# Performance work log

Hardware: AMD Instinct MI355X
Metric: run time of the kernel (lower is better)

## Reference

```python
import jax, jax.numpy as jnp
import numpy as np

D_MODEL = 1024
N_HEADS = 16
D_K = D_MODEL // N_HEADS
WINDOW = 512
ROPE_BASE = 10000.0


def _apply_rope(x):
    # x: [B, H, S, D] ; torchtune-style interleaved-pair RoPE
    S, D = x.shape[2], x.shape[3]
    half = D // 2
    inv_freq = 1.0 / (ROPE_BASE ** (jnp.arange(half, dtype=jnp.float32) / half))
    ang = jnp.arange(S, dtype=jnp.float32)[:, None] * inv_freq[None, :]  # [S, half]
    cos = jnp.cos(ang).astype(x.dtype)  # [S, half]
    sin = jnp.sin(ang).astype(x.dtype)
    x_even = x[..., ::2]   # [B,H,S,half]
    x_odd = x[..., 1::2]
    out_even = x_even * cos - x_odd * sin
    out_odd = x_odd * cos + x_even * sin
    return jnp.stack([out_even, out_odd], axis=-1).reshape(x.shape)


def setup_inputs() -> dict:
    key = jax.random.key(0)
    k1, k2, k3 = jax.random.split(key, 3)
    B, S = 2, 2048
    x = jax.random.normal(k1, (B, S, D_MODEL), dtype=jnp.float32)
    # store weights pre-transposed so y = x @ w (same math as nn.Linear)
    w_qkv = jax.random.normal(k2, (D_MODEL, 3 * D_MODEL), dtype=jnp.float32) * (D_MODEL ** -0.5)
    w_o = jax.random.normal(k3, (D_MODEL, D_MODEL), dtype=jnp.float32) * (D_MODEL ** -0.5)
    return {"x": x, "w_qkv": w_qkv, "w_o": w_o}


def reference(x, w_qkv, w_o):
    B, S, _ = x.shape
    qkv = (x @ w_qkv).reshape(B, S, 3, N_HEADS, D_K)
    qkv = jnp.transpose(qkv, (2, 0, 3, 1, 4))  # [3, B, H, S, Dk]
    q, k, v = qkv[0], qkv[1], qkv[2]
    q = _apply_rope(q)
    k = _apply_rope(k)
    # causal sliding-window mask: token i attends to j in [i - WINDOW, i]
    i = jnp.arange(S)[:, None]
    j = jnp.arange(S)[None, :]
    allowed = (j <= i) & (j >= i - WINDOW)
    bias = jnp.where(allowed, 0.0, -jnp.inf).astype(x.dtype)  # [S, S]
    scores = jnp.einsum('bhqd,bhkd->bhqk', q, k) * (D_K ** -0.5) + bias
    attn = jax.nn.softmax(scores, axis=-1)
    out = jnp.einsum('bhqk,bhkd->bhqd', attn, v)  # [B,H,S,Dk]
    out = jnp.transpose(out, (0, 2, 1, 3)).reshape(B, S, D_MODEL)
    return out @ w_o
```

## Files before the change

### kernel.cpp

```cpp
#include <hip/hip_runtime.h>
#include <hip/hip_bf16.h>
#include <math.h>

typedef __bf16 bhalf;
typedef __bf16 bhalf8 __attribute__((ext_vector_type(8)));
typedef float floatx4 __attribute__((ext_vector_type(4)));
typedef _Float16 fh;
typedef _Float16 half4 __attribute__((ext_vector_type(4)));

#define MFMA_BF16(A, B, C) __builtin_amdgcn_mfma_f32_16x16x32_bf16((A), (B), (C), 0, 0, 0)
#define MFMA_F16_K16(A, B, C) __builtin_amdgcn_mfma_f32_16x16x16f16((A), (B), (C), 0, 0, 0)

__device__ inline unsigned short bfb(float f) {
  union { bhalf h; unsigned short u; } c;
  c.h = (bhalf)f;
  return c.u;
}
__device__ inline unsigned short fhb(float f) {
  union { fh h; unsigned short u; } c;
  c.h = (fh)f;
  return c.u;
}

__device__ inline void gload_lds16(const void* g, void* l) {
  typedef const __attribute__((address_space(1))) unsigned int GU;
  typedef __attribute__((address_space(3))) unsigned int LU;
  __builtin_amdgcn_global_load_lds((GU*)g, (LU*)l, 16, 0, 0);
}

__global__ __launch_bounds__(256) void cvt_x_kernel(const float* __restrict__ in,
                                                    bhalf* __restrict__ out) {
  int i = (blockIdx.x * 256 + threadIdx.x) * 8;
  floatx4 v0 = *(const floatx4*)(in + i);
  floatx4 v1 = *(const floatx4*)(in + i + 4);
  bhalf8 o;
  o[0] = (bhalf)v0[0]; o[1] = (bhalf)v0[1]; o[2] = (bhalf)v0[2]; o[3] = (bhalf)v0[3];
  o[4] = (bhalf)v1[0]; o[5] = (bhalf)v1[1]; o[6] = (bhalf)v1[2]; o[7] = (bhalf)v1[3];
  *(bhalf8*)(out + i) = o;
}

__global__ __launch_bounds__(256) void transpose_bf_kernel(const float* __restrict__ in,
                                                           bhalf* __restrict__ out,
                                                           int R, int C) {
  __shared__ float tile[32][33];
  int c0 = blockIdx.x * 32, r0 = blockIdx.y * 32;
  int tx = threadIdx.x, ty = threadIdx.y;
#pragma unroll
  for (int i = 0; i < 32; i += 8)
    tile[ty + i][tx] = in[(size_t)(r0 + ty + i) * C + c0 + tx];
  __syncthreads();
#pragma unroll
  for (int i = 0; i < 32; i += 8)
    out[(size_t)(c0 + ty + i) * R + r0 + tx] = (bhalf)tile[tx][ty + i];
}

template <int EPI, int TN>
__global__ __launch_bounds__(256, 2) void gemm_bt_kernel(
    const bhalf* __restrict__ A, const bhalf* __restrict__ BT, float* __restrict__ Cout,
    bhalf* __restrict__ qb, bhalf* __restrict__ kb, fh* __restrict__ vb,
    int M, int N, int K) {
  constexpr int NT = TN / 32;
  __shared__ __attribute__((aligned(16))) bhalf As[128 * 32];
  __shared__ __attribute__((aligned(16))) bhalf Bs[TN * 32];
  const int tid = threadIdx.x;
  const int lane = tid & 63;
  const int w = tid >> 6, wr = w >> 1, wc = w & 1;
  const int m0 = blockIdx.y * 128, n0 = blockIdx.x * TN;
  const int l15 = lane & 15, lhi = lane >> 4;

  floatx4 acc[4][NT];
#pragma unroll
  for (int i = 0; i < 4; ++i)
#pragma unroll
    for (int j = 0; j < NT; ++j) acc[i][j] = (floatx4){0.f, 0.f, 0.f, 0.f};

  const int srow16 = lane >> 2;
  const int scg = (lane & 3) ^ ((lane >> 3) & 3);
  const bhalf* aP0 = A + (size_t)(m0 + 32 * w + srow16) * K + scg * 8;
  const bhalf* aP1 = aP0 + (size_t)16 * K;
  const bhalf* bP0 = BT + (size_t)(n0 + ((TN == 128) ? 32 * w : 16 * w) + srow16) * K + scg * 8;
  const bhalf* bP1 = bP0 + (size_t)16 * K;
  bhalf* aL0 = &As[(2 * w) * 512];
  bhalf* aL1 = &As[(2 * w + 1) * 512];
  bhalf* bL0 = (TN == 128) ? &Bs[(2 * w) * 512] : &Bs[w * 512];
  bhalf* bL1 = (TN == 128) ? &Bs[(2 * w + 1) * 512] : nullptr;

  const int fro = (l15 * 4 + (lhi ^ ((l15 >> 1) & 3))) * 8;

  for (int k0 = 0; k0 < K; k0 += 32) {
    __syncthreads();
    gload_lds16(aP0 + k0, aL0);
    gload_lds16(aP1 + k0, aL1);
    gload_lds16(bP0 + k0, bL0);
    if constexpr (TN == 128) gload_lds16(bP1 + k0, bL1);
    __syncthreads();
    bhalf8 af[4], bf[NT];
#pragma unroll
    for (int mt = 0; mt < 4; ++mt)
      af[mt] = *(const bhalf8*)&As[(wr * 4 + mt) * 512 + fro];
#pragma unroll
    for (int nt = 0; nt < NT; ++nt)
      bf[nt] = *(const bhalf8*)&Bs[(wc * NT + nt) * 512 + fro];
#pragma unroll
    for (int mt = 0; mt < 4; ++mt)
#pragma unroll
      for (int nt = 0; nt < NT; ++nt)
        acc[mt][nt] = MFMA_BF16(af[mt], bf[nt], acc[mt][nt]);
  }

  if constexpr (EPI == 0) {
#pragma unroll
    for (int mt = 0; mt < 4; ++mt)
#pragma unroll
      for (int nt = 0; nt < NT; ++nt)
#pragma unroll
        for (int r = 0; r < 4; ++r) {
          int mg = m0 + wr * 64 + mt * 16 + lhi * 4 + r;
          int ng = n0 + wc * (TN / 2) + nt * 16 + l15;
          Cout[(size_t)mg * N + ng] = acc[mt][nt][r];
        }
  } else {
    const int sel = n0 >> 10;
    if (sel == 2) {
#pragma unroll
      for (int mt = 0; mt < 4; ++mt) {
        int mg = m0 + wr * 64 + mt * 16 + lhi * 4;
        int b = mg >> 11, s0 = mg & 2047;
#pragma unroll
        for (int nt = 0; nt < NT; ++nt) {
          int ng = n0 + wc * (TN / 2) + nt * 16 + l15;
          int h = (ng & 1023) >> 6, d = ng & 63;
          union { unsigned short u[4]; uint2 v2; } pk;
#pragma unroll
          for (int r = 0; r < 4; ++r) pk.u[r] = fhb(acc[mt][nt][r]);
          *(uint2*)&vb[((size_t)((b << 4) + h) * 64 + d) * 2048 + s0] = pk.v2;
        }
      }
    } else {
      bhalf* dst = sel ? kb : qb;
#pragma unroll
      for (int nt = 0; nt < NT; ++nt) {
        int ng = n0 + wc * (TN / 2) + nt * 16 + l15;
        int h = (ng & 1023) >> 6, d = ng & 63;
        float inv = exp2f((float)(d >> 1) * -0.4152410118609203f);
#pragma unroll
        for (int mt = 0; mt < 4; ++mt) {
          int mg = m0 + wr * 64 + mt * 16 + lhi * 4;
          int b = mg >> 11, s0 = mg & 2047;
#pragma unroll
          for (int r = 0; r < 4; ++r) {
            float val = acc[mt][nt][r];
            float partner = __shfl_xor(val, 1, 64);
            if (!(l15 & 1)) {
              float ang = (float)(s0 + r) * inv;
              float sn = __sinf(ang), cs = __cosf(ang);
              float oe = cs * val - sn * partner;
              float oo = cs * partner + sn * val;
              unsigned int u = bfb(oe) | ((unsigned int)bfb(oo) << 16);
              *(unsigned int*)&dst[((size_t)((b << 4) + h) * 2048 + (s0 + r)) * 64 + d] = u;
            }
          }
        }
      }
    }
  }
}

__global__ __launch_bounds__(256, 4) void attn_kernel(const bhalf* __restrict__ qg,
                                                      const bhalf* __restrict__ kg,
                                                      const fh* __restrict__ vt,
                                                      bhalf* __restrict__ attn_out) {
  __shared__ __attribute__((aligned(16))) bhalf Ks[8 * 512];
  __shared__ __attribute__((aligned(16))) fh Vs[16 * 256];

  const int bh = blockIdx.x;
  const int bx = blockIdx.y;
  const int tid = threadIdx.x, lane = tid & 63, w = tid >> 6;
  const int l15 = lane & 15, quad = lane >> 4;
  const int q0 = bx * 64;
  const size_t base = (size_t)bh * 2048 * 64;
  const size_t vbase = (size_t)bh * 64 * 2048;

  bhalf8 qa0, qa1;
  {
    const bhalf* qp = qg + base + (size_t)(q0 + w * 16 + l15) * 64 + quad * 8;
    bhalf8 t0 = *(const bhalf8*)qp;
    bhalf8 t1 = *(const bhalf8*)(qp + 32);
#pragma unroll
    for (int j = 0; j < 8; ++j) {
      qa0[j] = (bhalf)((float)t0[j] * 0.18033688f);
      qa1[j] = (bhalf)((float)t1[j] * 0.18033688f);
    }
  }

  const int kf0 = 2 * w, kf1 = 2 * w + 1;
  const bhalf* kS0 = kg + base + (size_t)((kf0 >> 1) * 16 + (lane >> 2)) * 64 +
                     (kf0 & 1) * 32 + (lane & 3) * 8;
  const bhalf* kS1 = kg + base + (size_t)((kf1 >> 1) * 16 + (lane >> 2)) * 64 +
                     (kf1 & 1) * 32 + (lane & 3) * 8;
  const int vj0 = 2 * w, vj1 = 2 * w + 1;
  const int vfb0 = 2 * vj0 + (lane >> 5), vfb1 = 2 * vj1 + (lane >> 5);
  const fh* vS0 = vt + vbase + (size_t)((vfb0 & 3) * 16 + ((lane & 31) >> 1)) * 2048 +
                  w * 16 + (lane & 1) * 8;
  const fh* vS1 = vt + vbase + (size_t)((vfb1 & 3) * 16 + ((lane & 31) >> 1)) * 2048 +
                  w * 16 + (lane & 1) * 8;
  bhalf* kL0 = &Ks[kf0 * 512];
  bhalf* kL1 = &Ks[kf1 * 512];
  fh* vL0 = &Vs[vj0 * 512];
  fh* vL1 = &Vs[vj1 * 512];

  floatx4 O[4];
#pragma unroll
  for (int dt = 0; dt < 4; ++dt) O[dt] = (floatx4){0.f, 0.f, 0.f, 0.f};
  float lsum = 0.f;

  const int iG = q0 + w * 16 + l15;
  int kt0 = bx - 8;
  if (kt0 < 0) kt0 = 0;

  for (int kt = kt0; kt <= bx; ++kt) {
    __syncthreads();
    const size_t ko = (size_t)(kt * 64) * 64;
    const int vo = kt * 64;
    gload_lds16(kS0 + ko, kL0);
    gload_lds16(kS1 + ko, kL1);
    gload_lds16(vS0 + vo, vL0);
    gload_lds16(vS1 + vo, vL1);
    __syncthreads();

    floatx4 sf[4];
#pragma unroll
    for (int nt = 0; nt < 4; ++nt) {
      bhalf8 k0 = *(const bhalf8*)&Ks[(nt * 2) * 512 + (l15 * 4 + quad) * 8];
      bhalf8 k1 = *(const bhalf8*)&Ks[(nt * 2 + 1) * 512 + (l15 * 4 + quad) * 8];
      floatx4 s = (floatx4){0.f, 0.f, 0.f, 0.f};
      s = MFMA_BF16(k0, qa0, s);
      s = MFMA_BF16(k1, qa1, s);
      sf[nt] = s;
    }
    if (kt == bx) {
#pragma unroll
      for (int nt = 0; nt < 4; ++nt) {
        int jb = kt * 64 + nt * 16 + quad * 4;
#pragma unroll
        for (int r = 0; r < 4; ++r)
          if (jb + r > iG) sf[nt][r] = -1e30f;
      }
    } else if (kt == kt0 && bx >= 8) {
#pragma unroll
      for (int nt = 0; nt < 4; ++nt) {
        int jb = kt * 64 + nt * 16 + quad * 4;
#pragma unroll
        for (int r = 0; r < 4; ++r)
          if (jb + r + 512 < iG) sf[nt][r] = -1e30f;
      }
    }
#pragma unroll
    for (int nt = 0; nt < 4; ++nt) {
      half4 pf;
#pragma unroll
      for (int r = 0; r < 4; ++r) {
        float p = exp2f(sf[nt][r]);
        lsum += p;
        pf[r] = (fh)p;
      }
#pragma unroll
      for (int dt = 0; dt < 4; ++dt) {
        half4 vf = *(const half4*)&Vs[(nt * 4 + dt) * 256 + (l15 * 4 + quad) * 4];
        O[dt] = MFMA_F16_K16(vf, pf, O[dt]);
      }
    }
  }

  lsum += __shfl_xor(lsum, 16, 64);
  lsum += __shfl_xor(lsum, 32, 64);
  const float inv = 1.f / lsum;

  const int b = bh >> 4, h = bh & 15;
  const int s = q0 + w * 16 + l15;
#pragma unroll
  for (int dt = 0; dt < 4; ++dt) {
    union { unsigned short u[4]; uint2 v2; } pk;
#pragma unroll
    for (int r = 0; r < 4; ++r) pk.u[r] = bfb(O[dt][r] * inv);
    *(uint2*)&attn_out[(size_t)(b * 2048 + s) * 1024 + h * 64 + dt * 16 + quad * 4] = pk.v2;
  }
}

extern "C" void kernel_launch(void* const* d_in, const int* in_sizes, int n_in,
                              void* d_out, int out_size, void* d_ws, size_t ws_size,
                              hipStream_t stream) {
  (void)in_sizes; (void)n_in; (void)out_size; (void)ws_size;
  const float* x = (const float*)d_in[0];
  const float* w_qkv = (const float*)d_in[1];
  const float* w_o = (const float*)d_in[2];
  float* out = (float*)d_out;
  char* ws = (char*)d_ws;

  bhalf* x_bf  = (bhalf*)(ws);
  bhalf* wqkvT = (bhalf*)(ws + ((size_t)8 << 20));
  bhalf* woT   = (bhalf*)(ws + ((size_t)14 << 20));
  bhalf* qb    = (bhalf*)(ws + ((size_t)16 << 20));
  bhalf* kb    = (bhalf*)(ws + ((size_t)24 << 20));
  fh*    vb    = (fh*)(ws + ((size_t)32 << 20));
  bhalf* attn  = (bhalf*)(ws + ((size_t)40 << 20));

  cvt_x_kernel<<<2048, 256, 0, stream>>>(x, x_bf);
  transpose_bf_kernel<<<dim3(96, 32), dim3(32, 8), 0, stream>>>(w_qkv, wqkvT, 1024, 3072);
  transpose_bf_kernel<<<dim3(32, 32), dim3(32, 8), 0, stream>>>(w_o, woT, 1024, 1024);
  gemm_bt_kernel<1, 128><<<dim3(24, 32), 256, 0, stream>>>(x_bf, wqkvT, nullptr, qb, kb, vb,
                                                           4096, 3072, 1024);
  attn_kernel<<<dim3(32, 32), 256, 0, stream>>>(qb, kb, vb, attn);
  gemm_bt_kernel<0, 64><<<dim3(16, 32), 256, 0, stream>>>(attn, woT, out, nullptr, nullptr,
                                                          nullptr, 4096, 1024, 1024);
}
```

Baseline: 167.6 us.

## Merge weight transposes, deepen GEMM K-step, share KV tiles across two query tiles

The two weight-transpose launches become a single kernel launch. The GEMM K loop now stages 64-wide K slices per barrier pair, halving the number of syncs while doubling LDS use. The attention kernel processes two 64-row query tiles per block and stages two KV tiles per iteration, so each K/V tile is loaded once for both query tiles. This cuts global loads and barriers but halves the grid, doubles register state and lowers the occupancy hint from 4 to 2.

```diff
diff --git a/kernel.cpp b/kernel.cpp
--- a/kernel.cpp
+++ b/kernel.cpp
@@ -39,12 +39,19 @@
   *(bhalf8*)(out + i) = o;
 }
 
-__global__ __launch_bounds__(256) void transpose_bf_kernel(const float* __restrict__ in,
-                                                           bhalf* __restrict__ out,
-                                                           int R, int C) {
+__global__ __launch_bounds__(256) void transpose_w_kernel(const float* __restrict__ wqkv,
+                                                          const float* __restrict__ wo,
+                                                          bhalf* __restrict__ wqkvT,
+                                                          bhalf* __restrict__ woT) {
   __shared__ float tile[32][33];
-  int c0 = blockIdx.x * 32, r0 = blockIdx.y * 32;
-  int tx = threadIdx.x, ty = threadIdx.y;
+  const int bx = blockIdx.x;
+  const float* in = (bx < 96) ? wqkv : wo;
+  bhalf* out = (bx < 96) ? wqkvT : woT;
+  const int C = (bx < 96) ? 3072 : 1024;
+  const int cx = (bx < 96) ? bx : (bx - 96);
+  const int R = 1024;
+  int c0 = cx * 32, r0 = blockIdx.y * 32;
+  int tx = threadIdx.x & 31, ty = threadIdx.x >> 5;
 #pragma unroll
   for (int i = 0; i < 32; i += 8)
     tile[ty + i][tx] = in[(size_t)(r0 + ty + i) * C + c0 + tx];
@@ -60,8 +67,8 @@
     bhalf* __restrict__ qb, bhalf* __restrict__ kb, fh* __restrict__ vb,
     int M, int N, int K) {
   constexpr int NT = TN / 32;
-  __shared__ __attribute__((aligned(16))) bhalf As[128 * 32];
-  __shared__ __attribute__((aligned(16))) bhalf Bs[TN * 32];
+  __shared__ __attribute__((aligned(16))) bhalf As[128 * 64];
+  __shared__ __attribute__((aligned(16))) bhalf Bs[TN * 64];
   const int tid = threadIdx.x;
   const int lane = tid & 63;
   const int w = tid >> 6, wr = w >> 1, wc = w & 1;
@@ -87,25 +94,32 @@
 
   const int fro = (l15 * 4 + (lhi ^ ((l15 >> 1) & 3))) * 8;
 
-  for (int k0 = 0; k0 < K; k0 += 32) {
+  for (int k0 = 0; k0 < K; k0 += 64) {
     __syncthreads();
     gload_lds16(aP0 + k0, aL0);
     gload_lds16(aP1 + k0, aL1);
     gload_lds16(bP0 + k0, bL0);
     if constexpr (TN == 128) gload_lds16(bP1 + k0, bL1);
+    gload_lds16(aP0 + k0 + 32, aL0 + 4096);
+    gload_lds16(aP1 + k0 + 32, aL1 + 4096);
+    gload_lds16(bP0 + k0 + 32, bL0 + TN * 32);
+    if constexpr (TN == 128) gload_lds16(bP1 + k0 + 32, bL1 + TN * 32);
     __syncthreads();
-    bhalf8 af[4], bf[NT];
-#pragma unroll
-    for (int mt = 0; mt < 4; ++mt)
-      af[mt] = *(const bhalf8*)&As[(wr * 4 + mt) * 512 + fro];
-#pragma unroll
-    for (int nt = 0; nt < NT; ++nt)
-      bf[nt] = *(const bhalf8*)&Bs[(wc * NT + nt) * 512 + fro];
-#pragma unroll
-    for (int mt = 0; mt < 4; ++mt)
+#pragma unroll
+    for (int kh = 0; kh < 2; ++kh) {
+      bhalf8 af[4], bf[NT];
+#pragma unroll
+      for (int mt = 0; mt < 4; ++mt)
+        af[mt] = *(const bhalf8*)&As[kh * 4096 + (wr * 4 + mt) * 512 + fro];
 #pragma unroll
       for (int nt = 0; nt < NT; ++nt)
-        acc[mt][nt] = MFMA_BF16(af[mt], bf[nt], acc[mt][nt]);
+        bf[nt] = *(const bhalf8*)&Bs[kh * TN * 32 + (wc * NT + nt) * 512 + fro];
+#pragma unroll
+      for (int mt = 0; mt < 4; ++mt)
+#pragma unroll
+        for (int nt = 0; nt < NT; ++nt)
+          acc[mt][nt] = MFMA_BF16(af[mt], bf[nt], acc[mt][nt]);
+    }
   }
 
   if constexpr (EPI == 0) {
@@ -166,79 +180,71 @@
   }
 }
 
-__global__ __launch_bounds__(256, 4) void attn_kernel(const bhalf* __restrict__ qg,
+__global__ __launch_bounds__(256, 2) void attn_kernel(const bhalf* __restrict__ qg,
                                                       const bhalf* __restrict__ kg,
                                                       const fh* __restrict__ vt,
                                                       bhalf* __restrict__ attn_out) {
-  __shared__ __attribute__((aligned(16))) bhalf Ks[8 * 512];
-  __shared__ __attribute__((aligned(16))) fh Vs[16 * 256];
+  __shared__ __attribute__((aligned(16))) bhalf Ks[2][8 * 512];
+  __shared__ __attribute__((aligned(16))) fh Vs[2][16 * 256];
 
   const int bh = blockIdx.x;
-  const int bx = blockIdx.y;
+  const int qt2 = blockIdx.y;
   const int tid = threadIdx.x, lane = tid & 63, w = tid >> 6;
   const int l15 = lane & 15, quad = lane >> 4;
-  const int q0 = bx * 64;
+  const int q0 = qt2 * 128;
+  const int qtile0 = qt2 * 2;
   const size_t base = (size_t)bh * 2048 * 64;
   const size_t vbase = (size_t)bh * 64 * 2048;
 
-  bhalf8 qa0, qa1;
-  {
-    const bhalf* qp = qg + base + (size_t)(q0 + w * 16 + l15) * 64 + quad * 8;
+  bhalf8 qa[2][2];
+#pragma unroll
+  for (int h = 0; h < 2; ++h) {
+    const bhalf* qp = qg + base + (size_t)(q0 + h * 64 + w * 16 + l15) * 64 + quad * 8;
     bhalf8 t0 = *(const bhalf8*)qp;
     bhalf8 t1 = *(const bhalf8*)(qp + 32);
 #pragma unroll
     for (int j = 0; j < 8; ++j) {
-      qa0[j] = (bhalf)((float)t0[j] * 0.18033688f);
-      qa1[j] = (bhalf)((float)t1[j] * 0.18033688f);
-    }
-  }
-
-  const int kf0 = 2 * w, kf1 = 2 * w + 1;
-  const bhalf* kS0 = kg + base + (size_t)((kf0 >> 1) * 16 + (lane >> 2)) * 64 +
-                     (kf0 & 1) * 32 + (lane & 3) * 8;
-  const bhalf* kS1 = kg + base + (size_t)((kf1 >> 1) * 16 + (lane >> 2)) * 64 +
-                     (kf1 & 1) * 32 + (lane & 3) * 8;
-  const int vj0 = 2 * w, vj1 = 2 * w + 1;
-  const int vfb0 = 2 * vj0 + (lane >> 5), vfb1 = 2 * vj1 + (lane >> 5);
-  const fh* vS0 = vt + vbase + (size_t)((vfb0 & 3) * 16 + ((lane & 31) >> 1)) * 2048 +
-                  w * 16 + (lane & 1) * 8;
-  const fh* vS1 = vt + vbase + (size_t)((vfb1 & 3) * 16 + ((lane & 31) >> 1)) * 2048 +
-                  w * 16 + (lane & 1) * 8;
-  bhalf* kL0 = &Ks[kf0 * 512];
-  bhalf* kL1 = &Ks[kf1 * 512];
-  fh* vL0 = &Vs[vj0 * 512];
-  fh* vL1 = &Vs[vj1 * 512];
-
-  floatx4 O[4];
-#pragma unroll
-  for (int dt = 0; dt < 4; ++dt) O[dt] = (floatx4){0.f, 0.f, 0.f, 0.f};
-  float lsum = 0.f;
-
-  const int iG = q0 + w * 16 + l15;
-  int kt0 = bx - 8;
-  if (kt0 < 0) kt0 = 0;
-
-  for (int kt = kt0; kt <= bx; ++kt) {
-    __syncthreads();
-    const size_t ko = (size_t)(kt * 64) * 64;
-    const int vo = kt * 64;
-    gload_lds16(kS0 + ko, kL0);
-    gload_lds16(kS1 + ko, kL1);
-    gload_lds16(vS0 + vo, vL0);
-    gload_lds16(vS1 + vo, vL1);
-    __syncthreads();
-
+      qa[h][0][j] = (bhalf)((float)t0[j] * 0.18033688f);
+      qa[h][1][j] = (bhalf)((float)t1[j] * 0.18033688f);
+    }
+  }
+
+  const int kOff = (w * 16 + (lane >> 2)) * 64 + (lane & 3) * 8;
+  const int vfb0 = 4 * w + (lane >> 5), vfb1 = 4 * w + 2 + (lane >> 5);
+  const int vOff0 = ((vfb0 & 3) * 16 + ((lane & 31) >> 1)) * 2048 + w * 16 + (lane & 1) * 8;
+  const int vOff1 = ((vfb1 & 3) * 16 + ((lane & 31) >> 1)) * 2048 + w * 16 + (lane & 1) * 8;
+
+  floatx4 O[2][4];
+#pragma unroll
+  for (int h = 0; h < 2; ++h)
+#pragma unroll
+    for (int dt = 0; dt < 4; ++dt) O[h][dt] = (floatx4){0.f, 0.f, 0.f, 0.f};
+  float lsum[2] = {0.f, 0.f};
+
+  auto stage = [&](int kt, int buf) {
+    const bhalf* kp = kg + base + (size_t)(kt * 64) * 64 + kOff;
+    gload_lds16(kp, &Ks[buf][(2 * w) * 512]);
+    gload_lds16(kp + 32, &Ks[buf][(2 * w + 1) * 512]);
+    const fh* vp = vt + vbase + kt * 64;
+    gload_lds16(vp + vOff0, &Vs[buf][(2 * w) * 512]);
+    gload_lds16(vp + vOff1, &Vs[buf][(2 * w + 1) * 512]);
+  };
+
+  auto proc = [&](int buf, int kt, int h) {
+    const int diag = qtile0 + h;
+    if (kt > diag || kt < diag - 8) return;
+    const int iG = q0 + h * 64 + w * 16 + l15;
     floatx4 sf[4];
 #pragma unroll
     for (int nt = 0; nt < 4; ++nt) {
-      bhalf8 k0 = *(const bhalf8*)&Ks[(nt * 2) * 512 + (l15 * 4 + quad) * 8];
-      bhalf8 k1 = *(const bhalf8*)&Ks[(nt * 2 + 1) * 512 + (l15 * 4 + quad) * 8];
+      bhalf8 k0 = *(const bhalf8*)&Ks[buf][(nt * 2) * 512 + (l15 * 4 + quad) * 8];
+      bhalf8 k1 = *(const bhalf8*)&Ks[buf][(nt * 2 + 1) * 512 + (l15 * 4 + quad) * 8];
       floatx4 s = (floatx4){0.f, 0.f, 0.f, 0.f};
-      s = MFMA_BF16(k0, qa0, s);
-      s = MFMA_BF16(k1, qa1, s);
+      s = MFMA_BF16(k0, qa[h][0], s);
+      s = MFMA_BF16(k1, qa[h][1], s);
       sf[nt] = s;
     }
-    if (kt == bx) {
+    if (kt == diag) {
 #pragma unroll
       for (int nt = 0; nt < 4; ++nt) {
         int jb = kt * 64 + nt * 16 + quad * 4;
@@ -246,7 +252,7 @@
         for (int r = 0; r < 4; ++r)
           if (jb + r > iG) sf[nt][r] = -1e30f;
       }
-    } else if (kt == kt0 && bx >= 8) {
+    } else if (kt == diag - 8) {
 #pragma unroll
       for (int nt = 0; nt < 4; ++nt) {
         int jb = kt * 64 + nt * 16 + quad * 4;
@@ -261,29 +267,49 @@
 #pragma unroll
       for (int r = 0; r < 4; ++r) {
         float p = exp2f(sf[nt][r]);
-        lsum += p;
+        lsum[h] += p;
         pf[r] = (fh)p;
       }
 #pragma unroll
       for (int dt = 0; dt < 4; ++dt) {
-        half4 vf = *(const half4*)&Vs[(nt * 4 + dt) * 256 + (l15 * 4 + quad) * 4];
-        O[dt] = MFMA_F16_K16(vf, pf, O[dt]);
-      }
-    }
-  }
-
-  lsum += __shfl_xor(lsum, 16, 64);
-  lsum += __shfl_xor(lsum, 32, 64);
-  const float inv = 1.f / lsum;
-
-  const int b = bh >> 4, h = bh & 15;
-  const int s = q0 + w * 16 + l15;
-#pragma unroll
-  for (int dt = 0; dt < 4; ++dt) {
-    union { unsigned short u[4]; uint2 v2; } pk;
-#pragma unroll
-    for (int r = 0; r < 4; ++r) pk.u[r] = bfb(O[dt][r] * inv);
-    *(uint2*)&attn_out[(size_t)(b * 2048 + s) * 1024 + h * 64 + dt * 16 + quad * 4] = pk.v2;
+        half4 vf = *(const half4*)&Vs[buf][(nt * 4 + dt) * 256 + (l15 * 4 + quad) * 4];
+        O[h][dt] = MFMA_F16_K16(vf, pf, O[h][dt]);
+      }
+    }
+  };
+
+  int ktstart = qtile0 - 8;
+  if (ktstart < 0) ktstart = 0;
+  const int ktend = qtile0 + 1;
+  for (int kt = ktstart; kt <= ktend; kt += 2) {
+    const bool two = (kt + 1 <= ktend);
+    __syncthreads();
+    stage(kt, 0);
+    if (two) stage(kt + 1, 1);
+    __syncthreads();
+    proc(0, kt, 0);
+    proc(0, kt, 1);
+    if (two) {
+      proc(1, kt + 1, 0);
+      proc(1, kt + 1, 1);
+    }
+  }
+
+  const int b = bh >> 4, hh = bh & 15;
+#pragma unroll
+  for (int h = 0; h < 2; ++h) {
+    float t = lsum[h];
+    t += __shfl_xor(t, 16, 64);
+    t += __shfl_xor(t, 32, 64);
+    const float inv = 1.f / t;
+    const int s = q0 + h * 64 + w * 16 + l15;
+#pragma unroll
+    for (int dt = 0; dt < 4; ++dt) {
+      union { unsigned short u[4]; uint2 v2; } pk;
+#pragma unroll
+      for (int r = 0; r < 4; ++r) pk.u[r] = bfb(O[h][dt][r] * inv);
+      *(uint2*)&attn_out[(size_t)(b * 2048 + s) * 1024 + hh * 64 + dt * 16 + quad * 4] = pk.v2;
+    }
   }
 }
 
@@ -306,11 +332,10 @@
   bhalf* attn  = (bhalf*)(ws + ((size_t)40 << 20));
 
   cvt_x_kernel<<<2048, 256, 0, stream>>>(x, x_bf);
-  transpose_bf_kernel<<<dim3(96, 32), dim3(32, 8), 0, stream>>>(w_qkv, wqkvT, 1024, 3072);
-  transpose_bf_kernel<<<dim3(32, 32), dim3(32, 8), 0, stream>>>(w_o, woT, 1024, 1024);
+  transpose_w_kernel<<<dim3(128, 32), 256, 0, stream>>>(w_qkv, w_o, wqkvT, woT);
   gemm_bt_kernel<1, 128><<<dim3(24, 32), 256, 0, stream>>>(x_bf, wqkvT, nullptr, qb, kb, vb,
                                                            4096, 3072, 1024);
-  attn_kernel<<<dim3(32, 32), 256, 0, stream>>>(qb, kb, vb, attn);
+  attn_kernel<<<dim3(32, 16), 256, 0, stream>>>(qb, kb, vb, attn);
   gemm_bt_kernel<0, 64><<<dim3(16, 32), 256, 0, stream>>>(attn, woT, out, nullptr, nullptr,
                                                           nullptr, 4096, 1024, 1024);
 }
```

After: 162.4 us. 1.03x faster.
